# Optimization experiments

Hardware: AMD Instinct MI355X
Metric: run time of the kernel (lower is better)

Reference implementation:

```python
import jax, jax.numpy as jnp
import numpy as np

PAD = 2
STRIDE = 1

def _cayley(sig):
    # Geometric-product Cayley table G[i, j, k]: e_i * e_j = G[i, j, i^j] e_{i^j}
    # Blades indexed by bitmask over generators; sig = metric signature (+1/-1 per generator).
    n = len(sig)
    dim = 1 << n
    G = np.zeros((dim, dim, dim), dtype=np.float32)
    for a in range(dim):
        for b in range(dim):
            s = 0
            aa = a >> 1
            while aa:
                s += bin(aa & b).count('1')
                aa >>= 1
            sign = -1.0 if (s & 1) else 1.0
            common = a & b
            for i, m in enumerate(sig):
                if (common >> i) & 1:
                    sign *= m
            G[a, b, a ^ b] = sign
    return G


def setup_inputs() -> dict:
    key = jax.random.key(0)
    k1, k2, k3 = jax.random.split(key, 3)
    B, C, O, BD, L, K = 8, 64, 64, 8, 4096, 5
    x = jax.random.normal(k1, (B, C, BD, L), dtype=jnp.float32)
    bound = 1.0 / np.sqrt(C * BD * K)  # kaiming-style uniform bound
    W = jax.random.uniform(k2, (K, C, O, BD), minval=-bound, maxval=bound, dtype=jnp.float32)
    b = jax.random.uniform(k3, (1, O, BD, 1), minval=-bound, maxval=bound, dtype=jnp.float32)
    G = jnp.asarray(_cayley((1.0, 1.0, 1.0)))  # Cl(3,0), basis_dim = 8
    return {"x": x, "W": W, "b": b, "G": G}


def reference(x, W, b, G):
    # Original: pad length dim, unfold windows, then
    # result[b,o,k,w] = sum_{i,j,c,v} G[i,j,k] * W[v,c,o,i] * x_pad[b,c,j,w+v], plus bias.
    # Equivalent efficient form: pre-contract G with W into a conv kernel over
    # fused (channel, basis) axes and run a standard 1D convolution.
    K = W.shape[0]
    B, C, J, L = x.shape
    O = W.shape[2]
    Kb = G.shape[2]
    xp = jnp.pad(x, ((0, 0), (0, 0), (0, 0), (PAD, PAD)))  # padding_mode='zeros'
    # T[o,k,c,j,v] = sum_i G[i,j,k] W[v,c,o,i]  (tiny tensor: O*Kb x C*J x K)
    kern = jnp.einsum('ijk,vcoi->okcjv', G, W).reshape(O * Kb, C * J, K)
    xin = xp.reshape(B, C * J, L + 2 * PAD)
    out = jax.lax.conv_general_dilated(
        xin, kern, window_strides=(STRIDE,), padding='VALID',
        dimension_numbers=('NCH', 'OIH', 'NCH'))
    # out channels are (o major, k minor) per the reshape above
    return out.reshape(B, O, Kb, out.shape[-1]) + b
```

## Files before the change

### kernel.cpp

```cpp
#include <hip/hip_runtime.h>


#define C_    64
#define L_    4096
#define PAD_  2
#define OKch  512
#define KD_   2560

#define BM    128
#define BN    128
#define BKCJ  64
#define NCJB  8
#define NV    5
#define TILE  8192
#define ASTR  72
#define WIN   132

typedef __bf16 bf16x8 __attribute__((ext_vector_type(8)));
typedef float floatx4 __attribute__((ext_vector_type(4)));

__device__ __forceinline__ unsigned short f2bf(float f) {
    unsigned int u = __float_as_uint(f);
    u += 0x7FFFu + ((u >> 16) & 1u);
    return (unsigned short)(u >> 16);
}

__device__ __forceinline__ void glds16(const unsigned short* g, unsigned short* l) {
    __builtin_amdgcn_global_load_lds(
        (const __attribute__((address_space(1))) unsigned int*)(g),
        (__attribute__((address_space(3))) unsigned int*)(l),
        16, 0, 0);
}

#define WAIT_VMCNT_0()  asm volatile("s_waitcnt vmcnt(0)" ::: "memory")
#define WAIT_VMCNT_4()  asm volatile("s_waitcnt vmcnt(4)" ::: "memory")
#define WAIT_VMCNT_44() asm volatile("s_waitcnt vmcnt(44)" ::: "memory")
#define WAIT_LGKM_0()   asm volatile("s_waitcnt lgkmcnt(0)" ::: "memory")

__device__ __forceinline__ void barrier_raw() {
    asm volatile("" ::: "memory");
    __builtin_amdgcn_sched_barrier(0);
    __builtin_amdgcn_s_barrier();
    __builtin_amdgcn_sched_barrier(0);
    asm volatile("" ::: "memory");
}

__global__ __launch_bounds__(256) void build_kern(
    const float* __restrict__ W, const float* __restrict__ G,
    unsigned short* __restrict__ kernT)
{
    const int ok = blockIdx.y;
    const int kd = blockIdx.x * 256 + threadIdx.x;
    const int v  = kd >> 9;
    const int cj = kd & 511;
    const int c  = cj >> 3;
    const int j  = cj & 7;
    const int o  = ok >> 3;
    const int kb = ok & 7;
    const float* Wp = W + (((v * C_ + c) * 64 + o) << 3);
    const float4 w0 = *(const float4*)Wp;
    const float4 w1 = *(const float4*)(Wp + 4);
    const int gb = j * 8 + kb;
    float s = G[gb]       * w0.x + G[gb + 64]  * w0.y
            + G[gb + 128] * w0.z + G[gb + 192] * w0.w
            + G[gb + 256] * w1.x + G[gb + 320] * w1.y
            + G[gb + 384] * w1.z + G[gb + 448] * w1.w;
    const int y   = ok >> 7;
    const int m   = ok & 127;
    const int cjb = cj >> 6;
    const int kk  = cj & 63;
    kernT[(size_t)(((y * NCJB + cjb) * NV + v)) * TILE
          + m * 64 + (kk ^ ((m & 7) << 3))] = f2bf(s);
}

__device__ __forceinline__ void b_issue(const float* xb, int cj0, int w0,
                                        float br[5][8]) {
    const int tid = threadIdx.x;
    #pragma unroll
    for (int u = 0; u < 5; u++) {
        int idx; bool act;
        if (u < 4) { idx = u * 256 + tid; act = true; }
        else { act = ((tid & 7) == 0);
               idx = 1024 + ((tid >> 6) << 3) + ((tid >> 3) & 7); }
        if (act) {
            const int kgrp = idx / WIN;
            const int nn   = idx - kgrp * WIN;
            int ws = w0 - PAD_ + nn;
            ws = ws < 0 ? 0 : (ws > (L_ - 1) ? (L_ - 1) : ws);
            const float* xp = xb + ((size_t)(cj0 + (kgrp << 3)) << 12) + (size_t)ws;
            #pragma unroll
            for (int r = 0; r < 8; r++)
                br[u][r] = xp[(size_t)r << 12];
        }
    }
}

__device__ __forceinline__ void b_store(unsigned short* BsP, const float br[5][8],
                                        int w0) {
    const int tid = threadIdx.x;
    #pragma unroll
    for (int u = 0; u < 5; u++) {
        int idx; bool act;
        if (u < 4) { idx = u * 256 + tid; act = true; }
        else { act = ((tid & 7) == 0);
               idx = 1024 + ((tid >> 6) << 3) + ((tid >> 3) & 7); }
        if (act) {
            const int kgrp = idx / WIN;
            const int nn   = idx - kgrp * WIN;
            const bool inb = (unsigned)(w0 - PAD_ + nn) < (unsigned)L_;
            unsigned int pk[4];
            #pragma unroll
            for (int r = 0; r < 8; r++) {
                const unsigned short h = f2bf(inb ? br[u][r] : 0.0f);
                if (r & 1) pk[r >> 1] |= (unsigned int)h << 16;
                else       pk[r >> 1]  = h;
            }
            uint4 uu; uu.x = pk[0]; uu.y = pk[1]; uu.z = pk[2]; uu.w = pk[3];
            *reinterpret_cast<uint4*>(&BsP[nn * ASTR + (kgrp << 3)]) = uu;
        }
    }
}

__device__ __forceinline__ void a_stage(const unsigned short* tile,
                                        unsigned short* dst) {
    const int tid = threadIdx.x;
    #pragma unroll
    for (int u = 0; u < 4; u++) {
        const int e = (u * 256 + tid) << 3;
        glds16(tile + e, dst + e);
    }
}

__global__ __launch_bounds__(256, 2) void gpconv_mfma(
    const float* __restrict__ x, const unsigned short* __restrict__ kernT,
    const float* __restrict__ bias, float* __restrict__ out)
{
    __shared__ unsigned short As[2 * TILE];
    __shared__ unsigned short Bs[WIN * ASTR];

    const int tid  = threadIdx.x;
    const int lane = tid & 63;
    const int wave = tid >> 6;
    const int lrow = lane & 15;
    const int quad = lane >> 4;
    const int wm = (wave >> 1) << 6;
    const int wn = (wave & 1) << 6;

    const int bid = blockIdx.x;
    const int y   = (bid >> 3) & 3;
    const int xw  = ((bid >> 5) << 3) + (bid & 7);
    const int b   = xw >> 5;
    const int w0  = (xw & 31) * BN;
    const int mBase = y * BM;
    const float* xb = x + (size_t)b * (size_t)(512 * L_);
    const unsigned short* ky = kernT + (size_t)(y * NCJB) * NV * TILE;

    const int asw   = (lrow & 7) << 3;
    const int c0    = (quad << 3) ^ asw;
    const int c1    = (32 + (quad << 3)) ^ asw;
    const int arow0 = (wm + lrow) << 6;

    floatx4 acc[4][4];
    {
        const floatx4 z = {0.f, 0.f, 0.f, 0.f};
        #pragma unroll
        for (int i2 = 0; i2 < 4; i2++)
            #pragma unroll
            for (int j2 = 0; j2 < 4; j2++) acc[i2][j2] = z;
    }

    float br[5][8];

    b_issue(xb, 0, w0, br);
    a_stage(ky, As);
    WAIT_VMCNT_4();
    b_store(Bs, br, w0);
    __syncthreads();

    for (int cjb = 0; cjb < NCJB; cjb++) {
        const unsigned short* tcjb = ky + (size_t)cjb * NV * TILE;
        const bool last = (cjb == NCJB - 1);
        #pragma unroll
        for (int v = 0; v < NV; v++) {
            const int pv = (cjb & 1) ^ (v & 1);
            WAIT_LGKM_0();
            barrier_raw();
            if (v < 4)       a_stage(tcjb + (size_t)(v + 1) * TILE, &As[(pv ^ 1) * TILE]);
            else if (!last)  a_stage(tcjb + (size_t)NV * TILE,      &As[(pv ^ 1) * TILE]);
            if (v == 3 && !last) b_issue(xb, (cjb + 1) * BKCJ, w0, br);
            if ((v == 3 || v == 4) && !last) { WAIT_VMCNT_44(); }
            else if (v == 4 && last)         { WAIT_VMCNT_0();  }
            else                             { WAIT_VMCNT_4();  }
            barrier_raw();
            const unsigned short* Ab = &As[pv * TILE];
            #pragma unroll
            for (int kk2 = 0; kk2 < 2; kk2++) {
                const int cc = kk2 ? c1 : c0;
                bf16x8 af[4], bfr[4];
                #pragma unroll
                for (int mt = 0; mt < 4; mt++)
                    af[mt] = *reinterpret_cast<const bf16x8*>(
                        &Ab[arow0 + (mt << 10) + cc]);
                #pragma unroll
                for (int nt = 0; nt < 4; nt++)
                    bfr[nt] = *reinterpret_cast<const bf16x8*>(
                        &Bs[(wn + (nt << 4) + lrow + v) * ASTR + (kk2 << 5) + (quad << 3)]);
                __builtin_amdgcn_s_setprio(1);
                #pragma unroll
                for (int mt = 0; mt < 4; mt++)
                    #pragma unroll
                    for (int nt = 0; nt < 4; nt++)
                        acc[mt][nt] = __builtin_amdgcn_mfma_f32_16x16x32_bf16(
                            af[mt], bfr[nt], acc[mt][nt], 0, 0, 0);
                __builtin_amdgcn_s_setprio(0);
            }
        }
        if (!last) {
            WAIT_LGKM_0();
            barrier_raw();
            WAIT_VMCNT_4();
            b_store(Bs, br, w0);
            WAIT_LGKM_0();
        }
    }

    #pragma unroll
    for (int mt = 0; mt < 4; mt++) {
        #pragma unroll
        for (int e = 0; e < 4; e++) {
            const int okc = mBase + wm + (mt << 4) + (quad << 2) + e;
            const float bv = bias[okc];
            float* orow = out + ((size_t)b * OKch + (size_t)okc) * L_ + w0;
            #pragma unroll
            for (int nt = 0; nt < 4; nt++) {
                const int n = wn + (nt << 4) + lrow;
                orow[n] = acc[mt][nt][e] + bv;
            }
        }
    }
}

extern "C" void kernel_launch(void* const* d_in, const int* in_sizes, int n_in,
                              void* d_out, int out_size, void* d_ws, size_t ws_size,
                              hipStream_t stream) {
    const float* x    = (const float*)d_in[0];
    const float* W    = (const float*)d_in[1];
    const float* bias = (const float*)d_in[2];
    const float* G    = (const float*)d_in[3];
    unsigned short* kernT = (unsigned short*)d_ws;
    float* out = (float*)d_out;

    build_kern<<<dim3(KD_ / 256, OKch), 256, 0, stream>>>(W, G, kernT);
    gpconv_mfma<<<dim3(1024), 256, 0, stream>>>(x, kernT, bias, out);
}
```

Before: 208.5 us.

## Load A fragments directly into registers, dropping LDS staging of weights

The conv weight tile is now pre-laid out by build_kern in MFMA fragment order, so each lane loads its A operands straight from global memory into double-buffered registers instead of staging them through LDS with global_load_lds and barriers. The main loop is fully unrolled with register ping-pong prefetch, and the LDS A buffer plus most barriers and vmcnt waits are removed. build_kern also computes eight outputs per thread and writes them packed. This raises register pressure (two 8-vector A buffers alongside the x staging registers and accumulators) and relies on the compiler's own waitcnts for latency hiding. Each A element is also now re-read from global/L2 by every wave instead of once per block.

After: 184.9 us. -11.3%, faster.

```diff
diff --git a/kernel.cpp b/kernel.cpp
--- a/kernel.cpp
+++ b/kernel.cpp
@@ -25,17 +25,7 @@
     return (unsigned short)(u >> 16);
 }
 
-__device__ __forceinline__ void glds16(const unsigned short* g, unsigned short* l) {
-    __builtin_amdgcn_global_load_lds(
-        (const __attribute__((address_space(1))) unsigned int*)(g),
-        (__attribute__((address_space(3))) unsigned int*)(l),
-        16, 0, 0);
-}
-
-#define WAIT_VMCNT_0()  asm volatile("s_waitcnt vmcnt(0)" ::: "memory")
-#define WAIT_VMCNT_4()  asm volatile("s_waitcnt vmcnt(4)" ::: "memory")
-#define WAIT_VMCNT_44() asm volatile("s_waitcnt vmcnt(44)" ::: "memory")
-#define WAIT_LGKM_0()   asm volatile("s_waitcnt lgkmcnt(0)" ::: "memory")
+#define WAIT_LGKM_0() asm volatile("s_waitcnt lgkmcnt(0)" ::: "memory")
 
 __device__ __forceinline__ void barrier_raw() {
     asm volatile("" ::: "memory");
@@ -49,28 +39,42 @@
     const float* __restrict__ W, const float* __restrict__ G,
     unsigned short* __restrict__ kernT)
 {
-    const int ok = blockIdx.y;
-    const int kd = blockIdx.x * 256 + threadIdx.x;
-    const int v  = kd >> 9;
-    const int cj = kd & 511;
-    const int c  = cj >> 3;
-    const int j  = cj & 7;
-    const int o  = ok >> 3;
-    const int kb = ok & 7;
+    const int idx  = blockIdx.x * 256 + threadIdx.x;
+    const int lrow = idx & 15;
+    const int quad = (idx >> 4) & 3;
+    const int f    = (idx >> 6) & 15;
+    const int mq   = f >> 1;
+    const int kk2  = f & 1;
+    const int t    = idx >> 10;
+    const int v    = t % 5;
+    const int tc   = t / 5;
+    const int cjb  = tc & 7;
+    const int y    = tc >> 3;
+    const int m    = (mq << 4) | lrow;
+    const int ok   = (y << 7) | m;
+    const int o    = ok >> 3;
+    const int kb   = ok & 7;
+    const int c    = (cjb << 3) | (kk2 << 2) | quad;
+
     const float* Wp = W + (((v * C_ + c) * 64 + o) << 3);
     const float4 w0 = *(const float4*)Wp;
     const float4 w1 = *(const float4*)(Wp + 4);
-    const int gb = j * 8 + kb;
-    float s = G[gb]       * w0.x + G[gb + 64]  * w0.y
-            + G[gb + 128] * w0.z + G[gb + 192] * w0.w
-            + G[gb + 256] * w1.x + G[gb + 320] * w1.y
-            + G[gb + 384] * w1.z + G[gb + 448] * w1.w;
-    const int y   = ok >> 7;
-    const int m   = ok & 127;
-    const int cjb = cj >> 6;
-    const int kk  = cj & 63;
-    kernT[(size_t)(((y * NCJB + cjb) * NV + v)) * TILE
-          + m * 64 + (kk ^ ((m & 7) << 3))] = f2bf(s);
+    const float w[8] = {w0.x, w0.y, w0.z, w0.w, w1.x, w1.y, w1.z, w1.w};
+
+    unsigned int pk[4];
+    #pragma unroll
+    for (int j = 0; j < 8; j++) {
+        float s = 0.f;
+        #pragma unroll
+        for (int i = 0; i < 8; i++)
+            s += G[i * 64 + j * 8 + kb] * w[i];
+        const unsigned short h = f2bf(s);
+        if (j & 1) pk[j >> 1] |= (unsigned int)h << 16;
+        else       pk[j >> 1]  = h;
+    }
+    uint4 uu; uu.x = pk[0]; uu.y = pk[1]; uu.z = pk[2]; uu.w = pk[3];
+    *reinterpret_cast<uint4*>(
+        &kernT[((size_t)t << 13) + (f << 9) + (quad << 7) + (lrow << 3)]) = uu;
 }
 
 __device__ __forceinline__ void b_issue(const float* xb, int cj0, int w0,
@@ -121,13 +125,32 @@
     }
 }
 
-__device__ __forceinline__ void a_stage(const unsigned short* tile,
-                                        unsigned short* dst) {
-    const int tid = threadIdx.x;
-    #pragma unroll
-    for (int u = 0; u < 4; u++) {
-        const int e = (u * 256 + tid) << 3;
-        glds16(tile + e, dst + e);
+__device__ __forceinline__ void a_load(const unsigned short* t, int wb,
+                                       bf16x8 r[8]) {
+    #pragma unroll
+    for (int f = 0; f < 8; f++)
+        r[f] = *reinterpret_cast<const bf16x8*>(t + (f << 9) + wb);
+}
+
+__device__ __forceinline__ void compute_phase(
+    const bf16x8 a[8], const unsigned short* BsP,
+    int wn, int lrow, int quad, int v, floatx4 acc[4][4])
+{
+    #pragma unroll
+    for (int kk2 = 0; kk2 < 2; kk2++) {
+        bf16x8 bfr[4];
+        #pragma unroll
+        for (int nt = 0; nt < 4; nt++)
+            bfr[nt] = *reinterpret_cast<const bf16x8*>(
+                &BsP[(wn + (nt << 4) + lrow + v) * ASTR + (kk2 << 5) + (quad << 3)]);
+        __builtin_amdgcn_s_setprio(1);
+        #pragma unroll
+        for (int mt = 0; mt < 4; mt++)
+            #pragma unroll
+            for (int nt = 0; nt < 4; nt++)
+                acc[mt][nt] = __builtin_amdgcn_mfma_f32_16x16x32_bf16(
+                    a[mt * 2 + kk2], bfr[nt], acc[mt][nt], 0, 0, 0);
+        __builtin_amdgcn_s_setprio(0);
     }
 }
 
@@ -135,7 +158,6 @@
     const float* __restrict__ x, const unsigned short* __restrict__ kernT,
     const float* __restrict__ bias, float* __restrict__ out)
 {
-    __shared__ unsigned short As[2 * TILE];
     __shared__ unsigned short Bs[WIN * ASTR];
 
     const int tid  = threadIdx.x;
@@ -155,10 +177,7 @@
     const float* xb = x + (size_t)b * (size_t)(512 * L_);
     const unsigned short* ky = kernT + (size_t)(y * NCJB) * NV * TILE;
 
-    const int asw   = (lrow & 7) << 3;
-    const int c0    = (quad << 3) ^ asw;
-    const int c1    = (32 + (quad << 3)) ^ asw;
-    const int arow0 = (wm + lrow) << 6;
+    const int wb = wm * 64 + lane * 8;
 
     floatx4 acc[4][4];
     {
@@ -169,60 +188,52 @@
             for (int j2 = 0; j2 < 4; j2++) acc[i2][j2] = z;
     }
 
+    bf16x8 aX[8], aY[8];
     float br[5][8];
 
     b_issue(xb, 0, w0, br);
-    a_stage(ky, As);
-    WAIT_VMCNT_4();
+    a_load(ky, wb, aX);
     b_store(Bs, br, w0);
-    __syncthreads();
-
-    for (int cjb = 0; cjb < NCJB; cjb++) {
-        const unsigned short* tcjb = ky + (size_t)cjb * NV * TILE;
-        const bool last = (cjb == NCJB - 1);
-        #pragma unroll
-        for (int v = 0; v < NV; v++) {
-            const int pv = (cjb & 1) ^ (v & 1);
-            WAIT_LGKM_0();
-            barrier_raw();
-            if (v < 4)       a_stage(tcjb + (size_t)(v + 1) * TILE, &As[(pv ^ 1) * TILE]);
-            else if (!last)  a_stage(tcjb + (size_t)NV * TILE,      &As[(pv ^ 1) * TILE]);
-            if (v == 3 && !last) b_issue(xb, (cjb + 1) * BKCJ, w0, br);
-            if ((v == 3 || v == 4) && !last) { WAIT_VMCNT_44(); }
-            else if (v == 4 && last)         { WAIT_VMCNT_0();  }
-            else                             { WAIT_VMCNT_4();  }
-            barrier_raw();
-            const unsigned short* Ab = &As[pv * TILE];
-            #pragma unroll
-            for (int kk2 = 0; kk2 < 2; kk2++) {
-                const int cc = kk2 ? c1 : c0;
-                bf16x8 af[4], bfr[4];
-                #pragma unroll
-                for (int mt = 0; mt < 4; mt++)
-                    af[mt] = *reinterpret_cast<const bf16x8*>(
-                        &Ab[arow0 + (mt << 10) + cc]);
-                #pragma unroll
-                for (int nt = 0; nt < 4; nt++)
-                    bfr[nt] = *reinterpret_cast<const bf16x8*>(
-                        &Bs[(wn + (nt << 4) + lrow + v) * ASTR + (kk2 << 5) + (quad << 3)]);
-                __builtin_amdgcn_s_setprio(1);
-                #pragma unroll
-                for (int mt = 0; mt < 4; mt++)
-                    #pragma unroll
-                    for (int nt = 0; nt < 4; nt++)
-                        acc[mt][nt] = __builtin_amdgcn_mfma_f32_16x16x32_bf16(
-                            af[mt], bfr[nt], acc[mt][nt], 0, 0, 0);
-                __builtin_amdgcn_s_setprio(0);
-            }
-        }
-        if (!last) {
-            WAIT_LGKM_0();
-            barrier_raw();
-            WAIT_VMCNT_4();
-            b_store(Bs, br, w0);
-            WAIT_LGKM_0();
-        }
-    }
+    WAIT_LGKM_0();
+    barrier_raw();
+
+#define PHASE(CUR, NXT, CJB, V, DO_PRE, DO_BI, DO_ST)                        \
+    {                                                                        \
+        if (DO_PRE) a_load(ky + (size_t)((CJB) * 5 + (V) + 1) * TILE, wb, NXT); \
+        if (DO_BI)  b_issue(xb, ((CJB) + 1) * BKCJ, w0, br);                 \
+        compute_phase(CUR, Bs, wn, lrow, quad, (V), acc);                    \
+        if (DO_ST) {                                                         \
+            barrier_raw();                  \
+            b_store(Bs, br, w0);       \
+            WAIT_LGKM_0();                                                   \
+            barrier_raw();                           \
+        }                                                                    \
+    }
+
+    for (int cp = 0; cp < 3; cp++) {
+        const int c0 = cp * 2, c1 = c0 + 1;
+        PHASE(aX, aY, c0, 0, 1, 0, 0);
+        PHASE(aY, aX, c0, 1, 1, 0, 0);
+        PHASE(aX, aY, c0, 2, 1, 0, 0);
+        PHASE(aY, aX, c0, 3, 1, 1, 0);
+        PHASE(aX, aY, c0, 4, 1, 0, 1);
+        PHASE(aY, aX, c1, 0, 1, 0, 0);
+        PHASE(aX, aY, c1, 1, 1, 0, 0);
+        PHASE(aY, aX, c1, 2, 1, 0, 0);
+        PHASE(aX, aY, c1, 3, 1, 1, 0);
+        PHASE(aY, aX, c1, 4, 1, 0, 1);
+    }
+    PHASE(aX, aY, 6, 0, 1, 0, 0);
+    PHASE(aY, aX, 6, 1, 1, 0, 0);
+    PHASE(aX, aY, 6, 2, 1, 0, 0);
+    PHASE(aY, aX, 6, 3, 1, 1, 0);
+    PHASE(aX, aY, 6, 4, 1, 0, 1);
+    PHASE(aY, aX, 7, 0, 1, 0, 0);
+    PHASE(aX, aY, 7, 1, 1, 0, 0);
+    PHASE(aY, aX, 7, 2, 1, 0, 0);
+    PHASE(aX, aY, 7, 3, 1, 0, 0);
+    PHASE(aY, aX, 7, 4, 0, 0, 0);
+#undef PHASE
 
     #pragma unroll
     for (int mt = 0; mt < 4; mt++) {
@@ -250,6 +261,6 @@
     unsigned short* kernT = (unsigned short*)d_ws;
     float* out = (float*)d_out;
 
-    build_kern<<<dim3(KD_ / 256, OKch), 256, 0, stream>>>(W, G, kernT);
+    build_kern<<<dim3(640), 256, 0, stream>>>(W, G, kernT);
     gpconv_mfma<<<dim3(1024), 256, 0, stream>>>(x, kernT, bias, out);
 }
```
